# Performance work log

Hardware: AMD Instinct MI355X
Metric: run time of the kernel (lower is better)

## Reference

```python
import jax, jax.numpy as jnp
import numpy as np

DIM = 1024
N_HEADS = 16
HEAD_DIM = DIM // N_HEADS
B, T = 2, 2048


def setup_inputs() -> dict:
    key = jax.random.key(0)
    ks = jax.random.split(key, 6)
    x = jax.random.normal(ks[0], (B, T, DIM), dtype=jnp.float32)
    # causal 0/1 mask, broadcastable over batch and heads
    mask = jnp.tril(jnp.ones((T, T), dtype=jnp.int32))[None, None, :, :]
    s = 1.0 / np.sqrt(DIM)
    W_qkv = jax.random.normal(ks[1], (DIM, 3 * DIM), dtype=jnp.float32) * s
    b_qkv = jnp.zeros((3 * DIM,), dtype=jnp.float32)
    W_proj = jax.random.normal(ks[2], (DIM, DIM), dtype=jnp.float32) * s
    b_proj = jnp.zeros((DIM,), dtype=jnp.float32)
    return {"x": x, "W_qkv": W_qkv, "b_qkv": b_qkv, "W_proj": W_proj, "b_proj": b_proj, "mask": mask}


def reference(x, W_qkv, b_qkv, W_proj, b_proj, mask):
    Bx, Tx, C = x.shape
    qkv = x @ W_qkv + b_qkv  # [B,T,3C]
    q, k, v = jnp.split(qkv, 3, axis=-1)
    # [B,T,C] -> [B,H,T,Dh]
    def split_heads(t):
        return t.reshape(Bx, Tx, N_HEADS, HEAD_DIM).transpose(0, 2, 1, 3)
    q, k, v = split_heads(q), split_heads(k), split_heads(v)
    att = jnp.einsum('bhqd,bhkd->bhqk', q, k) / jnp.sqrt(jnp.float32(HEAD_DIM))
    att = jnp.where(mask == 0, jnp.float32(-jnp.inf), att)
    att = jax.nn.softmax(att, axis=-1)
    # dropout is identity in eval mode
    out = jnp.einsum('bhqk,bhkd->bhqd', att, v)
    out = out.transpose(0, 2, 1, 3).reshape(Bx, Tx, C)
    return out @ W_proj + b_proj
```

## Files before the change

### kernel.cpp

```cpp
#include <hip/hip_runtime.h>
#include <hip/hip_bf16.h>
#include <stdint.h>

#define DIM   1024
#define NHEAD 16
#define HD    64
#define SEQ   2048
#define NTOK  4096
#define QKV_REGION (NTOK * DIM)

typedef short          bf16x8 __attribute__((ext_vector_type(8)));
typedef float          f32x4  __attribute__((ext_vector_type(4)));
typedef float          f32x16 __attribute__((ext_vector_type(16)));
typedef unsigned short u16x8  __attribute__((ext_vector_type(8)));
typedef unsigned short u16x4  __attribute__((ext_vector_type(4)));

__device__ __forceinline__ unsigned short f2bf(float f) {
  union { float f; unsigned u; } x; x.f = f;
  unsigned r = x.u + 0x7FFFu + ((x.u >> 16) & 1u);
  return (unsigned short)(r >> 16);
}

__device__ __forceinline__ unsigned pack2bf(float a, float b) {
  return (unsigned)f2bf(a) | ((unsigned)f2bf(b) << 16);
}

__device__ __forceinline__ void gld16(void* lds, const void* g) {
  __builtin_amdgcn_global_load_lds(
      (const __attribute__((address_space(1))) unsigned int*)g,
      (__attribute__((address_space(3))) unsigned int*)lds, 16, 0, 0);
}

__global__ __launch_bounds__(256) void k_cvt(const float* __restrict__ in,
                                             unsigned short* __restrict__ out) {
  size_t i = ((size_t)blockIdx.x * 256 + threadIdx.x) * 8;
  float4 a = *(const float4*)(in + i);
  float4 b = *(const float4*)(in + i + 4);
  u16x8 o;
  o[0] = f2bf(a.x); o[1] = f2bf(a.y); o[2] = f2bf(a.z); o[3] = f2bf(a.w);
  o[4] = f2bf(b.x); o[5] = f2bf(b.y); o[6] = f2bf(b.z); o[7] = f2bf(b.w);
  *(u16x8*)(out + i) = o;
}

__global__ __launch_bounds__(256) void k_tr_f32bf16(const float* __restrict__ in,
                                                    unsigned short* __restrict__ out,
                                                    int R, int C) {
  __shared__ unsigned short t[64][72];
  int r0 = blockIdx.y * 64, c0 = blockIdx.x * 64;
  int tid = threadIdx.x;
  int rr = tid >> 4, cc = (tid & 15) * 4;
#pragma unroll
  for (int p = 0; p < 4; p++) {
    int r = p * 16 + rr;
    float4 v = *(const float4*)(in + (size_t)(r0 + r) * C + c0 + cc);
    t[r][cc + 0] = f2bf(v.x); t[r][cc + 1] = f2bf(v.y);
    t[r][cc + 2] = f2bf(v.z); t[r][cc + 3] = f2bf(v.w);
  }
  __syncthreads();
#pragma unroll
  for (int p = 0; p < 4; p++) {
    int c = p * 16 + rr;
    u16x4 v;
    v[0] = t[cc + 0][c]; v[1] = t[cc + 1][c];
    v[2] = t[cc + 2][c]; v[3] = t[cc + 3][c];
    *(u16x4*)(out + (size_t)(c0 + c) * R + r0 + cc) = v;
  }
}

__global__ __launch_bounds__(256) void k_tr_v(const unsigned short* __restrict__ v,
                                              unsigned short* __restrict__ vt) {
  __shared__ unsigned short s[64][72];
  int bh = blockIdx.y, t0 = blockIdx.x * 64;
  const unsigned short* in = v + (size_t)bh * SEQ * HD + (size_t)t0 * HD;
  unsigned short* out = vt + (size_t)bh * HD * SEQ + t0;
  int tid = threadIdx.x;
  int rr = tid >> 3, cc = (tid & 7) * 8;
#pragma unroll
  for (int p = 0; p < 2; p++) {
    int r = p * 32 + rr;
    u16x8 x = *(const u16x8*)(in + r * HD + cc);
#pragma unroll
    for (int j = 0; j < 8; j++) s[r][cc + j] = x[j];
  }
  __syncthreads();
#pragma unroll
  for (int p = 0; p < 2; p++) {
    int d = p * 32 + rr;
    u16x8 o;
#pragma unroll
    for (int j = 0; j < 8; j++) o[j] = s[cc + j][d];
    *(u16x8*)(out + (size_t)d * SEQ + cc) = o;
  }
}

template <int EPI>
__global__ __launch_bounds__(256) void k_gemm_bt(const unsigned short* __restrict__ A,
                                                 const unsigned short* __restrict__ Bt,
                                                 const float* __restrict__ bias,
                                                 void* __restrict__ Cout,
                                                 int M, int N, int K) {
  __shared__ unsigned short Al[2][128 * 64];
  __shared__ unsigned short Bl[2][128 * 64];
  const int tid = threadIdx.x, lane = tid & 63, w = tid >> 6;
  const int wm = w >> 1, wn = w & 1;
  const int nwg = gridDim.x * gridDim.y;
  const int id  = blockIdx.y * gridDim.x + blockIdx.x;
  const int swz = (id & 7) * (nwg >> 3) + (id >> 3);
  const int m0 = (swz / gridDim.x) * 128, n0 = (swz % gridDim.x) * 128;
  const f32x4 fzero = {0.f, 0.f, 0.f, 0.f};

  f32x4 acc[4][4];
#pragma unroll
  for (int m = 0; m < 4; m++)
#pragma unroll
    for (int n = 0; n < 4; n++) acc[m][n] = fzero;

#define GSTAGE(K0, BUF)                                                              \
  {                                                                                  \
    _Pragma("unroll")                                                                \
    for (int i = 0; i < 4; i++) {                                                    \
      int row = w * 32 + i * 8 + (lane >> 3);                                        \
      int ch = (lane & 7) ^ (row & 7);                                               \
      gld16(&Al[BUF][(w * 32 + i * 8) * 64], A + (size_t)(m0 + row) * K + (K0) + ch * 8); \
      gld16(&Bl[BUF][(w * 32 + i * 8) * 64], Bt + (size_t)(n0 + row) * K + (K0) + ch * 8);\
    }                                                                                \
  }

  GSTAGE(0, 0);
  for (int k0 = 0; k0 < K; k0 += 64) {
    const int buf = (k0 >> 6) & 1;
    __syncthreads();
    if (k0 + 64 < K) GSTAGE(k0 + 64, buf ^ 1);
#pragma unroll
    for (int ks = 0; ks < 2; ks++) {
      bf16x8 af[4], bfr[4];
#pragma unroll
      for (int m = 0; m < 4; m++) {
        int row = wm * 64 + m * 16 + (lane & 15);
        int ch = (ks * 4 + (lane >> 4)) ^ (row & 7);
        af[m] = *(const bf16x8*)&Al[buf][row * 64 + ch * 8];
      }
#pragma unroll
      for (int n = 0; n < 4; n++) {
        int row = wn * 64 + n * 16 + (lane & 15);
        int ch = (ks * 4 + (lane >> 4)) ^ (row & 7);
        bfr[n] = *(const bf16x8*)&Bl[buf][row * 64 + ch * 8];
      }
      __builtin_amdgcn_s_setprio(1);
#pragma unroll
      for (int m = 0; m < 4; m++)
#pragma unroll
        for (int n = 0; n < 4; n++)
          acc[m][n] = __builtin_amdgcn_mfma_f32_16x16x32_bf16(af[m], bfr[n], acc[m][n], 0, 0, 0);
      __builtin_amdgcn_s_setprio(0);
    }
  }
#undef GSTAGE

#pragma unroll
  for (int m = 0; m < 4; m++) {
#pragma unroll
    for (int n = 0; n < 4; n++) {
      int col = n0 + wn * 64 + n * 16 + (lane & 15);
      float bv = bias[col];
#pragma unroll
      for (int r = 0; r < 4; r++) {
        int row = m0 + wm * 64 + m * 16 + (lane >> 4) * 4 + r;
        float val = acc[m][n][r] + bv;
        if (EPI == 1) {
          ((float*)Cout)[(size_t)row * N + col] = val;
        } else {
          unsigned short* dst = (unsigned short*)Cout;
          int reg = col >> 10, nn = col & 1023;
          if (reg == 0) val *= 0.18033688011112042f;
          int h = nn >> 6, d = nn & 63;
          int b = row >> 11, t = row & 2047;
          size_t idx = (size_t)reg * QKV_REGION +
                       ((size_t)(b * NHEAD + h) * SEQ + t) * HD + d;
          dst[idx] = f2bf(val);
        }
      }
    }
  }
}

__global__ __launch_bounds__(512, 4) void k_attn(const unsigned short* __restrict__ Q,
                                                 const unsigned short* __restrict__ K,
                                                 const unsigned short* __restrict__ Vt,
                                                 unsigned short* __restrict__ O) {
  __shared__ unsigned short kl[2][2][64 * 64];
  __shared__ unsigned short vl[2][2][64 * 64];
  __shared__ float ml2[256];
  const int tid = threadIdx.x, lane = tid & 63, w = tid >> 6;
  const int hl = lane >> 5, q32 = lane & 31;
  const bool hb = (hl != 0);
  const int h = w >> 2, wr = w & 3;
  const int id = blockIdx.x;
  const int bh = id & 31;
  const int qt = (id < 256) ? (15 - (id >> 5)) : ((id >> 5) - 8);
  const unsigned short* Qb = Q + (size_t)bh * SEQ * HD;
  const unsigned short* Kb = K + (size_t)bh * SEQ * HD;
  const unsigned short* Vb = Vt + (size_t)bh * HD * SEQ;

  const int wq = qt * 128 + wr * 32;
  const int qmax = wq + 31;
  const int qg = wq + q32;
  const int nlo = qt + 1;
  const int kt0 = h ? nlo : 0;

  bf16x8 qf[4];
  {
    const unsigned short* qp = Qb + (size_t)(wq + q32) * HD + hl * 8;
#pragma unroll
    for (int ks = 0; ks < 4; ks++) qf[ks] = *(const bf16x8*)(qp + ks * 16);
  }

  f32x16 oacc[2];
#pragma unroll
  for (int nd = 0; nd < 2; nd++)
#pragma unroll
    for (int r = 0; r < 16; r++) oacc[nd][r] = 0.f;
  float mrun = -1e30f, lpart = 0.f;

#define ASTAGE(S, BUF)                                                                   \
  if ((S) < nlo) {                                                                       \
    const int kb_ = (kt0 + (S)) * 64;                                                    \
    _Pragma("unroll")                                                                    \
    for (int i = 0; i < 2; i++) {                                                        \
      int row = wr * 16 + i * 8 + (lane >> 3);                                           \
      int ch = (lane & 7) ^ (row & 7);                                                   \
      gld16(&kl[h][BUF][(wr * 16 + i * 8) * 64], Kb + (size_t)(kb_ + row) * HD + ch * 8);\
      gld16(&vl[h][BUF][(wr * 16 + i * 8) * 64], Vb + (size_t)row * SEQ + kb_ + ch * 8); \
    }                                                                                    \
  }

  ASTAGE(0, 0);
  __syncthreads();
  int cur = 0;

  for (int s = 0; s < nlo; s++) {
    ASTAGE(s + 1, cur ^ 1);
    const int kb = (kt0 + s) * 64;
    if (kb <= qmax) {
      f32x16 sacc[2];
#pragma unroll
      for (int nk = 0; nk < 2; nk++)
#pragma unroll
        for (int r = 0; r < 16; r++) sacc[nk][r] = 0.f;
      __builtin_amdgcn_s_setprio(1);
#pragma unroll
      for (int ks = 0; ks < 4; ks++) {
#pragma unroll
        for (int nk = 0; nk < 2; nk++) {
          int krow = nk * 32 + q32;
          int ch = (2 * ks + hl) ^ (krow & 7);
          bf16x8 kf = *(const bf16x8*)&kl[h][cur][krow * 64 + ch * 8];
          sacc[nk] = __builtin_amdgcn_mfma_f32_32x32x16_bf16(kf, qf[ks], sacc[nk], 0, 0, 0);
        }
      }
      __builtin_amdgcn_s_setprio(0);

      const bool nm = (kb + 63 > wq);
      if (nm) {
        const int kvbase = kb + hl * 4;
#pragma unroll
        for (int nk = 0; nk < 2; nk++)
#pragma unroll
          for (int rg = 0; rg < 4; rg++)
#pragma unroll
            for (int ri = 0; ri < 4; ri++) {
              int kv = kvbase + nk * 32 + rg * 8 + ri;
              if (kv > qg) sacc[nk][rg * 4 + ri] = -__builtin_inff();
            }
      }

      float tm[8];
#pragma unroll
      for (int i = 0; i < 8; i++)
        tm[i] = fmaxf(fmaxf(sacc[0][i], sacc[0][i + 8]),
                      fmaxf(sacc[1][i], sacc[1][i + 8]));
#pragma unroll
      for (int i = 0; i < 4; i++) tm[i] = fmaxf(tm[i], tm[i + 4]);
      float rmax = fmaxf(fmaxf(tm[0], tm[2]), fmaxf(tm[1], tm[3]));
      rmax = fmaxf(rmax, __shfl_xor(rmax, 32));

      if (!__all(rmax <= mrun + 8.0f)) {
        float mnew = fmaxf(mrun, rmax);
        float fac = exp2f(mrun - mnew);
        mrun = mnew;
        lpart *= fac;
#pragma unroll
        for (int rg = 0; rg < 4; rg++)
#pragma unroll
          for (int ri = 0; ri < 4; ri++) {
            float fr = __shfl(fac, ri + rg * 8 + hl * 4);
            oacc[0][rg * 4 + ri] *= fr;
            oacc[1][rg * 4 + ri] *= fr;
          }
      }

#pragma unroll
      for (int nk = 0; nk < 2; nk++)
#pragma unroll
        for (int r = 0; r < 16; r++)
          sacc[nk][r] = exp2f(sacc[nk][r] - mrun);
      {
        float ts[8];
#pragma unroll
        for (int i = 0; i < 8; i++)
          ts[i] = (sacc[0][i] + sacc[0][i + 8]) + (sacc[1][i] + sacc[1][i + 8]);
#pragma unroll
        for (int i = 0; i < 4; i++) ts[i] = ts[i] + ts[i + 4];
        lpart += (ts[0] + ts[2]) + (ts[1] + ts[3]);
      }

#pragma unroll
      for (int nk = 0; nk < 2; nk++) {
        unsigned cc[4][2];
#pragma unroll
        for (int m = 0; m < 4; m++) {
          cc[m][0] = pack2bf(sacc[nk][4 * m + 0], sacc[nk][4 * m + 1]);
          cc[m][1] = pack2bf(sacc[nk][4 * m + 2], sacc[nk][4 * m + 3]);
        }
        unsigned rv[2][2];
#pragma unroll
        for (int mm = 0; mm < 2; mm++) {
          unsigned sx = hb ? cc[2 * mm][0] : cc[2 * mm + 1][0];
          unsigned sy = hb ? cc[2 * mm][1] : cc[2 * mm + 1][1];
          rv[mm][0] = (unsigned)__shfl_xor((int)sx, 32);
          rv[mm][1] = (unsigned)__shfl_xor((int)sy, 32);
        }
        __builtin_amdgcn_s_setprio(1);
#pragma unroll
        for (int sl = 0; sl < 2; sl++) {
          const int me = 2 * sl;
          union { bf16x8 v; unsigned u[4]; } A;
          A.u[0] = hb ? rv[sl][0] : cc[me][0];
          A.u[1] = hb ? rv[sl][1] : cc[me][1];
          A.u[2] = hb ? cc[me + 1][0] : rv[sl][0];
          A.u[3] = hb ? cc[me + 1][1] : rv[sl][1];
          const int ss = nk * 2 + sl;
#pragma unroll
          for (int nd = 0; nd < 2; nd++) {
            int vrow = nd * 32 + q32;
            int ch = (2 * ss + hl) ^ (vrow & 7);
            bf16x8 vf = *(const bf16x8*)&vl[h][cur][vrow * 64 + ch * 8];
            oacc[nd] = __builtin_amdgcn_mfma_f32_32x32x16_bf16(A.v, vf, oacc[nd], 0, 0, 0);
          }
        }
        __builtin_amdgcn_s_setprio(0);
      }
    }
    __syncthreads();
    cur ^= 1;
  }
#undef ASTAGE

  float lf = lpart + __shfl_xor(lpart, 32);
  float* o1 = (float*)&kl[0][0][0];
  if (h == 1) {
#pragma unroll
    for (int nd = 0; nd < 2; nd++)
#pragma unroll
      for (int rg = 0; rg < 4; rg++)
#pragma unroll
        for (int ri = 0; ri < 4; ri++) {
          int row = wr * 32 + ri + rg * 8 + hl * 4;
          o1[row * 64 + nd * 32 + q32] = oacc[nd][rg * 4 + ri];
        }
    if (lane < 32) {
      ml2[(wr * 32 + lane) * 2 + 0] = mrun;
      ml2[(wr * 32 + lane) * 2 + 1] = lf;
    }
  }
  __syncthreads();
  if (h == 0) {
    const int b = bh >> 4, hh = bh & 15;
    float m1 = ml2[(wr * 32 + q32) * 2 + 0];
    float l1 = ml2[(wr * 32 + q32) * 2 + 1];
    float ms = fmaxf(mrun, m1);
    float f0 = exp2f(mrun - ms), f1 = exp2f(m1 - ms);
    float inv = 1.f / (lf * f0 + l1 * f1);
    float a0 = f0 * inv, a1 = f1 * inv;
#pragma unroll
    for (int rg = 0; rg < 4; rg++)
#pragma unroll
      for (int ri = 0; ri < 4; ri++) {
        int srcl = ri + rg * 8 + hl * 4;
        float b0 = __shfl(a0, srcl);
        float b1 = __shfl(a1, srcl);
        int row = wr * 32 + srcl;
        int t = qt * 128 + row;
#pragma unroll
        for (int nd = 0; nd < 2; nd++) {
          int d = nd * 32 + q32;
          float val = oacc[nd][rg * 4 + ri] * b0 + o1[row * 64 + d] * b1;
          O[((size_t)(b * SEQ + t)) * DIM + hh * HD + d] = f2bf(val);
        }
      }
  }
}

extern "C" void kernel_launch(void* const* d_in, const int* in_sizes, int n_in,
                              void* d_out, int out_size, void* d_ws, size_t ws_size,
                              hipStream_t stream) {
  const float* x     = (const float*)d_in[0];
  const float* Wqkv  = (const float*)d_in[1];
  const float* bqkv  = (const float*)d_in[2];
  const float* Wproj = (const float*)d_in[3];
  const float* bproj = (const float*)d_in[4];
  float* out = (float*)d_out;

  unsigned short* ws     = (unsigned short*)d_ws;
  unsigned short* xb_vt  = ws;
  unsigned short* wqkvt  = xb_vt + 4194304;
  unsigned short* wprojt = wqkvt + 3145728;
  unsigned short* q      = wprojt + 1048576;
  unsigned short* k      = q + 4194304;
  unsigned short* v_o    = k + 4194304;

  k_cvt<<<2048, 256, 0, stream>>>(x, xb_vt);
  k_tr_f32bf16<<<dim3(48, 16), 256, 0, stream>>>(Wqkv, wqkvt, 1024, 3072);
  k_tr_f32bf16<<<dim3(16, 16), 256, 0, stream>>>(Wproj, wprojt, 1024, 1024);
  k_gemm_bt<0><<<dim3(24, 32), 256, 0, stream>>>(xb_vt, wqkvt, bqkv, q, NTOK, 3072, DIM);
  k_tr_v<<<dim3(32, 32), 256, 0, stream>>>(v_o, xb_vt);
  k_attn<<<dim3(512), 512, 0, stream>>>(q, k, xb_vt, v_o);
  k_gemm_bt<1><<<dim3(8, 32), 256, 0, stream>>>(v_o, wprojt, bproj, out, NTOK, DIM, DIM);
}
```

Measured before the change: 131.8 us.

## Merge prep kernels, simplify GEMM to single buffer, truncate P to bf16

Combines the x conversion and both weight transposes into one launch to cut launch overhead. The GEMM loses its LDS double-buffering, tile swizzle and setprio hints and now loads each K-slice, syncs, then computes. The attention kernel packs probabilities to bf16 by truncation rather than round-to-nearest, which saves ALU work but adds rounding bias. The GEMM change exposes global load latency and may hurt L2 locality.

Result: faster. 124.8 us (-5.4%).

```diff
diff --git a/kernel.cpp b/kernel.cpp
--- a/kernel.cpp
+++ b/kernel.cpp
@@ -21,8 +21,9 @@
   return (unsigned short)(r >> 16);
 }
 
-__device__ __forceinline__ unsigned pack2bf(float a, float b) {
-  return (unsigned)f2bf(a) | ((unsigned)f2bf(b) << 16);
+__device__ __forceinline__ unsigned pack2bf_tr(float a, float b) {
+  union { float f; unsigned u; } x, y; x.f = a; y.f = b;
+  return (x.u >> 16) | (y.u & 0xFFFF0000u);
 }
 
 __device__ __forceinline__ void gld16(void* lds, const void* g) {
@@ -31,23 +32,29 @@
       (__attribute__((address_space(3))) unsigned int*)lds, 16, 0, 0);
 }
 
-__global__ __launch_bounds__(256) void k_cvt(const float* __restrict__ in,
-                                             unsigned short* __restrict__ out) {
-  size_t i = ((size_t)blockIdx.x * 256 + threadIdx.x) * 8;
-  float4 a = *(const float4*)(in + i);
-  float4 b = *(const float4*)(in + i + 4);
-  u16x8 o;
-  o[0] = f2bf(a.x); o[1] = f2bf(a.y); o[2] = f2bf(a.z); o[3] = f2bf(a.w);
-  o[4] = f2bf(b.x); o[5] = f2bf(b.y); o[6] = f2bf(b.z); o[7] = f2bf(b.w);
-  *(u16x8*)(out + i) = o;
-}
-
-__global__ __launch_bounds__(256) void k_tr_f32bf16(const float* __restrict__ in,
-                                                    unsigned short* __restrict__ out,
-                                                    int R, int C) {
+__global__ __launch_bounds__(256) void k_prep(const float* __restrict__ x,
+                                              unsigned short* __restrict__ xb,
+                                              const float* __restrict__ Wqkv,
+                                              unsigned short* __restrict__ wqkvt,
+                                              const float* __restrict__ Wproj,
+                                              unsigned short* __restrict__ wprojt) {
   __shared__ unsigned short t[64][72];
-  int r0 = blockIdx.y * 64, c0 = blockIdx.x * 64;
-  int tid = threadIdx.x;
+  const int bid = blockIdx.x, tid = threadIdx.x;
+  if (bid < 2048) {
+    size_t i = ((size_t)bid * 256 + tid) * 8;
+    float4 a = *(const float4*)(x + i);
+    float4 b = *(const float4*)(x + i + 4);
+    u16x8 o;
+    o[0] = f2bf(a.x); o[1] = f2bf(a.y); o[2] = f2bf(a.z); o[3] = f2bf(a.w);
+    o[4] = f2bf(b.x); o[5] = f2bf(b.y); o[6] = f2bf(b.z); o[7] = f2bf(b.w);
+    *(u16x8*)(xb + i) = o;
+    return;
+  }
+  const float* in; unsigned short* out; int C, bx, by;
+  if (bid < 2816) { in = Wqkv; out = wqkvt; C = 3072; bx = (bid - 2048) % 48; by = (bid - 2048) / 48; }
+  else            { in = Wproj; out = wprojt; C = 1024; bx = (bid - 2816) % 16; by = (bid - 2816) / 16; }
+  const int R = 1024;
+  int r0 = by * 64, c0 = bx * 64;
   int rr = tid >> 4, cc = (tid & 15) * 4;
 #pragma unroll
   for (int p = 0; p < 4; p++) {
@@ -99,14 +106,11 @@
                                                  const float* __restrict__ bias,
                                                  void* __restrict__ Cout,
                                                  int M, int N, int K) {
-  __shared__ unsigned short Al[2][128 * 64];
-  __shared__ unsigned short Bl[2][128 * 64];
+  __shared__ unsigned short Al[128 * 64];
+  __shared__ unsigned short Bl[128 * 64];
   const int tid = threadIdx.x, lane = tid & 63, w = tid >> 6;
   const int wm = w >> 1, wn = w & 1;
-  const int nwg = gridDim.x * gridDim.y;
-  const int id  = blockIdx.y * gridDim.x + blockIdx.x;
-  const int swz = (id & 7) * (nwg >> 3) + (id >> 3);
-  const int m0 = (swz / gridDim.x) * 128, n0 = (swz % gridDim.x) * 128;
+  const int m0 = blockIdx.y * 128, n0 = blockIdx.x * 128;
   const f32x4 fzero = {0.f, 0.f, 0.f, 0.f};
 
   f32x4 acc[4][4];
@@ -115,22 +119,16 @@
 #pragma unroll
     for (int n = 0; n < 4; n++) acc[m][n] = fzero;
 
-#define GSTAGE(K0, BUF)                                                              \
-  {                                                                                  \
-    _Pragma("unroll")                                                                \
-    for (int i = 0; i < 4; i++) {                                                    \
-      int row = w * 32 + i * 8 + (lane >> 3);                                        \
-      int ch = (lane & 7) ^ (row & 7);                                               \
-      gld16(&Al[BUF][(w * 32 + i * 8) * 64], A + (size_t)(m0 + row) * K + (K0) + ch * 8); \
-      gld16(&Bl[BUF][(w * 32 + i * 8) * 64], Bt + (size_t)(n0 + row) * K + (K0) + ch * 8);\
-    }                                                                                \
-  }
-
-  GSTAGE(0, 0);
   for (int k0 = 0; k0 < K; k0 += 64) {
-    const int buf = (k0 >> 6) & 1;
     __syncthreads();
-    if (k0 + 64 < K) GSTAGE(k0 + 64, buf ^ 1);
+#pragma unroll
+    for (int i = 0; i < 4; i++) {
+      int row = w * 32 + i * 8 + (lane >> 3);
+      int ch = (lane & 7) ^ (row & 7);
+      gld16(&Al[(w * 32 + i * 8) * 64], A + (size_t)(m0 + row) * K + k0 + ch * 8);
+      gld16(&Bl[(w * 32 + i * 8) * 64], Bt + (size_t)(n0 + row) * K + k0 + ch * 8);
+    }
+    __syncthreads();
 #pragma unroll
     for (int ks = 0; ks < 2; ks++) {
       bf16x8 af[4], bfr[4];
@@ -138,24 +136,21 @@
       for (int m = 0; m < 4; m++) {
         int row = wm * 64 + m * 16 + (lane & 15);
         int ch = (ks * 4 + (lane >> 4)) ^ (row & 7);
-        af[m] = *(const bf16x8*)&Al[buf][row * 64 + ch * 8];
+        af[m] = *(const bf16x8*)&Al[row * 64 + ch * 8];
       }
 #pragma unroll
       for (int n = 0; n < 4; n++) {
         int row = wn * 64 + n * 16 + (lane & 15);
         int ch = (ks * 4 + (lane >> 4)) ^ (row & 7);
-        bfr[n] = *(const bf16x8*)&Bl[buf][row * 64 + ch * 8];
-      }
-      __builtin_amdgcn_s_setprio(1);
+        bfr[n] = *(const bf16x8*)&Bl[row * 64 + ch * 8];
+      }
 #pragma unroll
       for (int m = 0; m < 4; m++)
 #pragma unroll
         for (int n = 0; n < 4; n++)
           acc[m][n] = __builtin_amdgcn_mfma_f32_16x16x32_bf16(af[m], bfr[n], acc[m][n], 0, 0, 0);
-      __builtin_amdgcn_s_setprio(0);
     }
   }
-#undef GSTAGE
 
 #pragma unroll
   for (int m = 0; m < 4; m++) {
@@ -319,8 +314,8 @@
         unsigned cc[4][2];
 #pragma unroll
         for (int m = 0; m < 4; m++) {
-          cc[m][0] = pack2bf(sacc[nk][4 * m + 0], sacc[nk][4 * m + 1]);
-          cc[m][1] = pack2bf(sacc[nk][4 * m + 2], sacc[nk][4 * m + 3]);
+          cc[m][0] = pack2bf_tr(sacc[nk][4 * m + 0], sacc[nk][4 * m + 1]);
+          cc[m][1] = pack2bf_tr(sacc[nk][4 * m + 2], sacc[nk][4 * m + 3]);
         }
         unsigned rv[2][2];
 #pragma unroll
@@ -419,9 +414,7 @@
   unsigned short* k      = q + 4194304;
   unsigned short* v_o    = k + 4194304;
 
-  k_cvt<<<2048, 256, 0, stream>>>(x, xb_vt);
-  k_tr_f32bf16<<<dim3(48, 16), 256, 0, stream>>>(Wqkv, wqkvt, 1024, 3072);
-  k_tr_f32bf16<<<dim3(16, 16), 256, 0, stream>>>(Wproj, wprojt, 1024, 1024);
+  k_prep<<<3072, 256, 0, stream>>>(x, xb_vt, Wqkv, wqkvt, Wproj, wprojt);
   k_gemm_bt<0><<<dim3(24, 32), 256, 0, stream>>>(xb_vt, wqkvt, bqkv, q, NTOK, 3072, DIM);
   k_tr_v<<<dim3(32, 32), 256, 0, stream>>>(v_o, xb_vt);
   k_attn<<<dim3(512), 512, 0, stream>>>(q, k, xb_vt, v_o);
```
